# Kernel optimization log

Measured on AMD Instinct MI355X. Metric: run time of the kernel, lower is better.

Reference implementation:

```python
import jax, jax.numpy as jnp
import numpy as np
from jax import lax

D = 1024          # channel / embedding dim
K = 2048          # codebook size
BN_EPS = 1e-5


def conv1d(x, w, b, stride):
    # x: [N, C, L], w: [O, I, k]
    y = lax.conv_general_dilated(x, w, window_strides=(stride,), padding='VALID',
                                 dimension_numbers=('NCH', 'OIH', 'NCH'))
    return y + b[None, :, None]


def batchnorm1d(x, gamma, beta):
    # training-mode BN: batch statistics over (N, L) per channel, biased variance
    mean = jnp.mean(x, axis=(0, 2), keepdims=True)
    var = jnp.var(x, axis=(0, 2), keepdims=True)
    return (x - mean) * lax.rsqrt(var + BN_EPS) * gamma[None, :, None] + beta[None, :, None]


def setup_inputs() -> dict:
    key = jax.random.key(0)
    ks = jax.random.split(key, 8)
    x = jax.random.normal(ks[0], (32, D, 1024), dtype=jnp.float32)
    conv1_w = jax.random.normal(ks[1], (D, D, 4), dtype=jnp.float32) * 0.02
    conv1_b = jnp.zeros((D,), dtype=jnp.float32)
    bn1_g = jnp.ones((D,), dtype=jnp.float32)
    bn1_b = jnp.zeros((D,), dtype=jnp.float32)
    conv2_w = jax.random.normal(ks[2], (D, D, 1), dtype=jnp.float32) * 0.02
    conv2_b = jnp.zeros((D,), dtype=jnp.float32)
    bn2_g = jnp.ones((D,), dtype=jnp.float32)
    bn2_b = jnp.zeros((D,), dtype=jnp.float32)
    codebook = jax.random.normal(ks[3], (K, D), dtype=jnp.float32)
    return {'x': x, 'conv1_w': conv1_w, 'conv1_b': conv1_b,
            'bn1_g': bn1_g, 'bn1_b': bn1_b,
            'conv2_w': conv2_w, 'conv2_b': conv2_b,
            'bn2_g': bn2_g, 'bn2_b': bn2_b,
            'codebook': codebook}


def encoder(x, conv1_w, conv1_b, bn1_g, bn1_b, conv2_w, conv2_b, bn2_g, bn2_b):
    h = conv1d(x, conv1_w, conv1_b, stride=2)           # [B, D, L']
    # ResidualWrapper(BN -> ReLU -> Conv1x1)
    r = batchnorm1d(h, bn1_g, bn1_b)
    r = jax.nn.relu(r)
    r = conv1d(r, conv2_w, conv2_b, stride=1)
    h = h + r
    h = batchnorm1d(h, bn2_g, bn2_b)
    return h


def vq(h, codebook):
    # axis=1 -> move channel axis last: [B, L', D]
    z = jnp.moveaxis(h, 1, -1)
    # squared Euclidean distances via ||z||^2 - 2 z.e + ||e||^2  (cdist+argmin)
    z2 = jnp.sum(z * z, axis=-1, keepdims=True)                  # [B, L', 1]
    e2 = jnp.sum(codebook * codebook, axis=-1)                   # [K]
    ze = jnp.einsum('bld,kd->blk', z, codebook)                  # [B, L', K]
    dist2 = z2 - 2.0 * ze + e2[None, None, :]
    ids = jnp.argmin(dist2, axis=-1)                             # [B, L'] int
    q = codebook[ids]                                            # [B, L', D]
    sg = lax.stop_gradient
    commitment = jnp.mean((z - sg(q)) ** 2)
    codebook_loss = jnp.mean((sg(z) - q) ** 2)
    # straight-through estimator
    q_st = z + sg(q - z)
    q_st = jnp.moveaxis(q_st, -1, 1)                             # back to [B, D, L']
    return q_st, ids, commitment, codebook_loss


def reference(x, conv1_w, conv1_b, bn1_g, bn1_b, conv2_w, conv2_b, bn2_g, bn2_b, codebook):
    h = encoder(x, conv1_w, conv1_b, bn1_g, bn1_b, conv2_w, conv2_b, bn2_g, bn2_b)
    q_st, ids, commitment, codebook_loss = vq(h, codebook)
    return q_st, ids, commitment, codebook_loss
```

## Files before the change

kernel.cpp:

```cpp
#include <hip/hip_runtime.h>
#include <hip/hip_bf16.h>
#include <cstdint>

#define DD 1024
#define LIN 1024
#define LP 511
#define LPAD 512
#define NBATCH 32
#define KCB 2048
#define BN_EPS 1e-5f

#define OUT_IDS 16744448u
#define OUT_LOSS 16760800u

#define WS_H1 0
#define WS_UNI 16777216
#define WS_XH  (WS_UNI)
#define WS_XL  (WS_UNI + 16777728)
#define WS_WTH (WS_UNI + 33555456)
#define WS_WTL (WS_UNI + 35652608)
#define WS_T2  (WS_UNI)
#define WS_RH  (WS_UNI + 16777216)
#define WS_RL  (WS_UNI + 25165824)
#define WS_ZH  WS_RH
#define WS_ZL  WS_RL
#define WS_W2H (WS_UNI + 33554432)
#define WS_W2L (WS_UNI + 34078720)
#define WS_CBH (WS_UNI + 34603008)
#define WS_CBL (WS_UNI + 35651584)
#define WS_AUX (WS_UNI + 37749760)
#define WS_A1 (WS_AUX + 0)
#define WS_B1 (WS_AUX + 1024)
#define WS_A2 (WS_AUX + 2048)
#define WS_B2 (WS_AUX + 3072)
#define WS_E2 (WS_AUX + 4096)
#define WS_SLOTS (WS_AUX + 6144)
#define WS_LOSS (WS_AUX + 6144 + 32704)

typedef __attribute__((ext_vector_type(8))) short bf16x8;
typedef __attribute__((ext_vector_type(4))) float f32x4;
typedef __attribute__((ext_vector_type(4))) unsigned short ushort4v;

__device__ __forceinline__ void async_cp16(const void* gsrc, void* ldst) {
  __builtin_amdgcn_global_load_lds(
      (const __attribute__((address_space(1))) unsigned int*)gsrc,
      (__attribute__((address_space(3))) unsigned int*)ldst, 16, 0, 0);
}

__device__ __forceinline__ void bf16split(float v, unsigned short& hi, unsigned short& lo) {
  __hip_bfloat16 h = __float2bfloat16(v);
  float hf = __bfloat162float(h);
  __hip_bfloat16 l = __float2bfloat16(v - hf);
  hi = *(unsigned short*)&h;
  lo = *(unsigned short*)&l;
}

__device__ inline float blockReduce256(float v, float* sb) {
#pragma unroll
  for (int off = 32; off > 0; off >>= 1) v += __shfl_down(v, off);
  __syncthreads();
  if ((threadIdx.x & 63) == 0) sb[threadIdx.x >> 6] = v;
  __syncthreads();
  return sb[0] + sb[1] + sb[2] + sb[3];
}

#define VMCNT(n) asm volatile("s_waitcnt vmcnt(" #n ")" ::: "memory")

template <typename SF>
__device__ __forceinline__ void stage_slot(const SF& sf, int c, int slot,
                                           unsigned short* smbase, int wid,
                                           int lane) {
  int plane, r0;
  if (slot < 4) {
    plane = 2 + (slot >> 1);
    r0 = ((slot & 1) << 7) + (wid << 4);
  } else {
    plane = wid & 1;
    r0 = (((wid >> 1) & 1) << 7) + ((slot - 4) << 5) + ((wid >> 2) << 4);
  }
  const unsigned short* g = sf(c, plane) + (size_t)(r0 + (lane >> 2)) * 1024 +
                            (((lane & 3) ^ ((lane >> 3) & 3)) << 3);
  unsigned short* d = smbase + plane * 8192 + r0 * 32;
  async_cp16(g, d);
}

template <typename SF>
__device__ __forceinline__ void mfma256_core(const SF& sf, unsigned short* sm,
                                             int nkc, f32x4 (&acc)[8][4]) {
  const int tid = threadIdx.x;
  const int wid = tid >> 6, lane = tid & 63;
  const int wm = wid >> 2, wn = wid & 3;
  const int slot16 = (((lane >> 4) ^ ((lane >> 1) & 3)) << 3);
  const int arow = (wm << 7) + (lane & 15);
  const int brow = (wn << 6) + (lane & 15);

#pragma unroll
  for (int s = 0; s < 8; ++s) stage_slot(sf, 0, s, sm, wid, lane);

  bf16x8 fbh[4], fbl[4];
  for (int c = 0; c < nkc; ++c) {
    unsigned short* buf = sm + ((c & 1) << 15);
    unsigned short* nbuf = sm + (((c + 1) & 1) << 15);
    const unsigned short* As = buf;
    const unsigned short* Als = buf + 8192;
    const unsigned short* Bs = buf + 16384;
    const unsigned short* Bls = buf + 24576;
    const bool pre = (c + 1 < nkc);
#pragma unroll
    for (int p = 0; p < 4; ++p) {
      if (pre) {
        if (p == 0) { VMCNT(3); } else if (p == 1) { VMCNT(4); }
        else if (p == 2) { VMCNT(5); } else { VMCNT(6); }
      } else {
        if (p == 0) { VMCNT(3); } else if (p == 1) { VMCNT(2); }
        else if (p == 2) { VMCNT(1); } else { VMCNT(0); }
      }
      __builtin_amdgcn_s_barrier();
      asm volatile("" ::: "memory");
      __builtin_amdgcn_sched_barrier(0);
      if (p == 0) {
#pragma unroll
        for (int nt = 0; nt < 4; ++nt) {
          int r = brow + nt * 16;
          fbh[nt] = *(const bf16x8*)(Bs + r * 32 + slot16);
          fbl[nt] = *(const bf16x8*)(Bls + r * 32 + slot16);
        }
      }
      bf16x8 fah0, fal0, fah1, fal1;
      {
        int r0 = arow + ((2 * p) << 4);
        int r1 = r0 + 16;
        fah0 = *(const bf16x8*)(As + r0 * 32 + slot16);
        fal0 = *(const bf16x8*)(Als + r0 * 32 + slot16);
        fah1 = *(const bf16x8*)(As + r1 * 32 + slot16);
        fal1 = *(const bf16x8*)(Als + r1 * 32 + slot16);
      }
      if (pre) {
        stage_slot(sf, c + 1, 2 * p + 0, nbuf, wid, lane);
        stage_slot(sf, c + 1, 2 * p + 1, nbuf, wid, lane);
      }
      __builtin_amdgcn_s_setprio(1);
#pragma unroll
      for (int nt = 0; nt < 4; ++nt) {
        acc[2 * p][nt] = __builtin_amdgcn_mfma_f32_16x16x32_bf16(fah0, fbh[nt], acc[2 * p][nt], 0, 0, 0);
        acc[2 * p][nt] = __builtin_amdgcn_mfma_f32_16x16x32_bf16(fah0, fbl[nt], acc[2 * p][nt], 0, 0, 0);
        acc[2 * p][nt] = __builtin_amdgcn_mfma_f32_16x16x32_bf16(fal0, fbh[nt], acc[2 * p][nt], 0, 0, 0);
      }
#pragma unroll
      for (int nt = 0; nt < 4; ++nt) {
        acc[2 * p + 1][nt] = __builtin_amdgcn_mfma_f32_16x16x32_bf16(fah1, fbh[nt], acc[2 * p + 1][nt], 0, 0, 0);
        acc[2 * p + 1][nt] = __builtin_amdgcn_mfma_f32_16x16x32_bf16(fah1, fbl[nt], acc[2 * p + 1][nt], 0, 0, 0);
        acc[2 * p + 1][nt] = __builtin_amdgcn_mfma_f32_16x16x32_bf16(fal1, fbh[nt], acc[2 * p + 1][nt], 0, 0, 0);
      }
      __builtin_amdgcn_s_setprio(0);
    }
  }
}

__global__ __launch_bounds__(256) void split_w1_kernel(
    const float* __restrict__ w, unsigned short* __restrict__ wth,
    unsigned short* __restrict__ wtl) {
  int idx = blockIdx.x * 256 + threadIdx.x;
  int o = idx >> 10, i = idx & 1023;
  float4 v = *(const float4*)&w[(size_t)idx * 4];
  float vv[4] = {v.x, v.y, v.z, v.w};
#pragma unroll
  for (int t = 0; t < 4; ++t) {
    unsigned short hi, lo;
    bf16split(vv[t], hi, lo);
    size_t off = (((size_t)(t << 10) + o) << 10) + i;
    wth[off] = hi;
    wtl[off] = lo;
  }
}

__global__ __launch_bounds__(256) void split_rows_kernel(
    const float* __restrict__ src, unsigned short* __restrict__ dsth,
    unsigned short* __restrict__ dstl) {
  size_t base = ((size_t)blockIdx.x * 256 + threadIdx.x) * 4;
  float4 v = *(const float4*)&src[base];
  float vv[4] = {v.x, v.y, v.z, v.w};
  ushort4v h, l;
#pragma unroll
  for (int j = 0; j < 4; ++j) {
    unsigned short hi, lo;
    bf16split(vv[j], hi, lo);
    h[j] = hi;
    l[j] = lo;
  }
  *(ushort4v*)&dsth[base] = h;
  *(ushort4v*)&dstl[base] = l;
}

__global__ __launch_bounds__(256) void split_x_kernel(
    const float* __restrict__ x, unsigned short* __restrict__ xh,
    unsigned short* __restrict__ xl) {
  __shared__ float lsT[128 * 65];
  const int l0 = blockIdx.x * 128;
  const int i0 = blockIdx.y * 64;
  const int nB = blockIdx.z;
  const int tid = threadIdx.x;
#pragma unroll
  for (int p = 0; p < 8; ++p) {
    int flat = p * 256 + tid;
    int row = flat >> 5, col4 = (flat & 31) * 4;
    float4 v = *(const float4*)&x[((size_t)nB * DD + i0 + row) * LIN + l0 + col4];
    lsT[(col4 + 0) * 65 + row] = v.x;
    lsT[(col4 + 1) * 65 + row] = v.y;
    lsT[(col4 + 2) * 65 + row] = v.z;
    lsT[(col4 + 3) * 65 + row] = v.w;
  }
  __syncthreads();
  const int lo2 = (l0 >> 1);
#pragma unroll
  for (int p = 0; p < 16; ++p) {
    int cp = p * 4 + (tid >> 6);
    int il = tid & 63;
    float vE = lsT[(2 * cp) * 65 + il];
    float vO = lsT[(2 * cp + 1) * 65 + il];
    unsigned short hE, lE, hO, lO;
    bf16split(vE, hE, lE);
    bf16split(vO, hO, lO);
    size_t dE = (((size_t)(0 * 32 + nB) * 512) + lo2 + cp) * 1024 + i0 + il;
    size_t dO = (((size_t)(1 * 32 + nB) * 512) + lo2 + cp) * 1024 + i0 + il;
    xh[dE] = hE; xl[dE] = lE;
    xh[dO] = hO; xl[dO] = lO;
  }
}

__global__ __launch_bounds__(256) void trans_affine_split_kernel(
    const float* __restrict__ src, const float* __restrict__ a,
    const float* __restrict__ b, unsigned short* __restrict__ dsth,
    unsigned short* __restrict__ dstl, int do_relu) {
  __shared__ float lsT[128 * 65];
  const int l0 = blockIdx.x * 128;
  const int i0 = blockIdx.y * 64;
  const int nB = blockIdx.z;
  const int tid = threadIdx.x;
#pragma unroll
  for (int p = 0; p < 8; ++p) {
    int flat = p * 256 + tid;
    int row = flat >> 5, col4 = (flat & 31) * 4;
    float4 v = *(const float4*)&src[((size_t)nB * DD + i0 + row) * LPAD + l0 + col4];
    lsT[(col4 + 0) * 65 + row] = v.x;
    lsT[(col4 + 1) * 65 + row] = v.y;
    lsT[(col4 + 2) * 65 + row] = v.z;
    lsT[(col4 + 3) * 65 + row] = v.w;
  }
  __syncthreads();
  const int il = tid & 63;
  const float ac = a[i0 + il], bc = b[i0 + il];
#pragma unroll
  for (int p = 0; p < 32; ++p) {
    int cp = p * 4 + (tid >> 6);
    float v = fmaf(ac, lsT[cp * 65 + il], bc);
    if (do_relu) v = fmaxf(v, 0.f);
    unsigned short hi, lo;
    bf16split(v, hi, lo);
    size_t d = (((size_t)nB * 512) + l0 + cp) * 1024 + i0 + il;
    dsth[d] = hi;
    dstl[d] = lo;
  }
}

__global__ __launch_bounds__(512, 2) void conv1_mfma_kernel(
    const unsigned short* __restrict__ wth, const unsigned short* __restrict__ wtl,
    const unsigned short* __restrict__ xh, const unsigned short* __restrict__ xl,
    const float* __restrict__ bias, float* __restrict__ h1) {
  extern __shared__ unsigned short sm[];
  const int tid = threadIdx.x;
  const int wid = tid >> 6, lane = tid & 63;
  const int lb = blockIdx.x * 256, ob = blockIdx.y * 256, nB = blockIdx.z;

  f32x4 acc[8][4];
#pragma unroll
  for (int a = 0; a < 8; ++a)
#pragma unroll
    for (int b = 0; b < 4; ++b) acc[a][b] = (f32x4){0.f, 0.f, 0.f, 0.f};

  auto sf = [&](int c, int plane) -> const unsigned short* {
    int t = c >> 5, kc = c & 31;
    if (plane == 0) return wth + ((((size_t)t << 10) + ob) << 10) + kc * 32;
    if (plane == 1) return wtl + ((((size_t)t << 10) + ob) << 10) + kc * 32;
    const unsigned short* xp = (plane == 2) ? xh : xl;
    return xp + ((((size_t)((t & 1) * 32 + nB) * 512) + lb + (t >> 1)) << 10) + kc * 32;
  };
  mfma256_core(sf, sm, 128, acc);

  const int wm = wid >> 2, wn = wid & 3;
#pragma unroll
  for (int mt = 0; mt < 8; ++mt) {
    const int o_base = ob + (wm << 7) + mt * 16 + ((lane >> 4) << 2);
#pragma unroll
    for (int nt = 0; nt < 4; ++nt) {
      const int l = lb + (wn << 6) + nt * 16 + (lane & 15);
      if (l < LP) {
#pragma unroll
        for (int rg = 0; rg < 4; ++rg)
          h1[((size_t)(nB << 10) + o_base + rg) * LPAD + l] =
              acc[mt][nt][rg] + bias[o_base + rg];
      }
    }
  }
}

__global__ __launch_bounds__(512, 2) void conv2_mfma_kernel(
    const unsigned short* __restrict__ w2h, const unsigned short* __restrict__ w2l,
    const unsigned short* __restrict__ rh, const unsigned short* __restrict__ rl,
    const float* __restrict__ b2c, const float* __restrict__ h1,
    float* __restrict__ t2) {
  extern __shared__ unsigned short sm[];
  const int tid = threadIdx.x;
  const int wid = tid >> 6, lane = tid & 63;
  const int lb = blockIdx.x * 256, ob = blockIdx.y * 256, nB = blockIdx.z;

  f32x4 acc[8][4];
#pragma unroll
  for (int a = 0; a < 8; ++a)
#pragma unroll
    for (int b = 0; b < 4; ++b) acc[a][b] = (f32x4){0.f, 0.f, 0.f, 0.f};

  auto sf = [&](int c, int plane) -> const unsigned short* {
    if (plane == 0) return w2h + ((size_t)ob << 10) + (size_t)c * 32;
    if (plane == 1) return w2l + ((size_t)ob << 10) + (size_t)c * 32;
    const unsigned short* rp = (plane == 2) ? rh : rl;
    return rp + (((size_t)nB * 512 + lb) << 10) + (size_t)c * 32;
  };
  mfma256_core(sf, sm, 32, acc);

  const int wm = wid >> 2, wn = wid & 3;
#pragma unroll
  for (int mt = 0; mt < 8; ++mt) {
    const int o_base = ob + (wm << 7) + mt * 16 + ((lane >> 4) << 2);
#pragma unroll
    for (int nt = 0; nt < 4; ++nt) {
      const int l = lb + (wn << 6) + nt * 16 + (lane & 15);
      if (l < LP) {
#pragma unroll
        for (int rg = 0; rg < 4; ++rg) {
          size_t off = ((size_t)(nB << 10) + o_base + rg) * LPAD + l;
          t2[off] = h1[off] + acc[mt][nt][rg] + b2c[o_base + rg];
        }
      }
    }
  }
}

__global__ __launch_bounds__(512, 2) void dist_mfma_kernel(
    const unsigned short* __restrict__ cbh, const unsigned short* __restrict__ cbl,
    const unsigned short* __restrict__ zh, const unsigned short* __restrict__ zl,
    const float* __restrict__ e2, unsigned long long* __restrict__ slots) {
  extern __shared__ unsigned short sm[];
  unsigned long long* best = (unsigned long long*)(sm + 65536);
  const int tid = threadIdx.x;
  const int wid = tid >> 6, lane = tid & 63;
  const int lb = blockIdx.x * 256, kb = blockIdx.y * 256, nB = blockIdx.z;

  if (tid < 256) best[tid] = ~0ULL;

  f32x4 acc[8][4];
#pragma unroll
  for (int a = 0; a < 8; ++a)
#pragma unroll
    for (int b = 0; b < 4; ++b) acc[a][b] = (f32x4){0.f, 0.f, 0.f, 0.f};

  auto sf = [&](int c, int plane) -> const unsigned short* {
    if (plane == 0) return cbh + ((size_t)kb << 10) + (size_t)c * 32;
    if (plane == 1) return cbl + ((size_t)kb << 10) + (size_t)c * 32;
    const unsigned short* zp = (plane == 2) ? zh : zl;
    return zp + (((size_t)nB * 512 + lb) << 10) + (size_t)c * 32;
  };
  mfma256_core(sf, sm, 32, acc);

  const int wm = wid >> 2, wn = wid & 3;
#pragma unroll
  for (int nt = 0; nt < 4; ++nt) {
    const int col = (wn << 6) + nt * 16 + (lane & 15);
    float dmin = 3.4e38f;
    int kmin = 0;
#pragma unroll
    for (int mt = 0; mt < 8; ++mt) {
      const int kbase = kb + (wm << 7) + mt * 16 + ((lane >> 4) << 2);
#pragma unroll
      for (int rg = 0; rg < 4; ++rg) {
        float dist = fmaf(-2.f, acc[mt][nt][rg], e2[kbase + rg]);
        if (dist < dmin) { dmin = dist; kmin = kbase + rg; }
      }
    }
    unsigned long long pk =
        ((unsigned long long)__float_as_uint(dmin) << 32) | (unsigned)kmin;
    atomicMin(&best[col], pk);
  }
  __syncthreads();
  if (tid < 256) {
    int l = lb + tid;
    if (l < LP) atomicMin(&slots[(size_t)nB * LP + l], best[tid]);
  }
}

__global__ __launch_bounds__(256) void bn_stats_kernel(
    const float* __restrict__ src, const float* __restrict__ gamma,
    const float* __restrict__ beta, float* __restrict__ a_out,
    float* __restrict__ b_out) {
  __shared__ float sb[4];
  const int c = blockIdx.x;
  const float* p = src + (size_t)c * LPAD;
  float s1 = 0.f, s2 = 0.f;
  for (int idx = threadIdx.x; idx < NBATCH * LP; idx += 256) {
    int nn = idx / LP;
    int l = idx - nn * LP;
    float v = p[(size_t)nn * DD * LPAD + l];
    s1 += v;
    s2 = fmaf(v, v, s2);
  }
  s1 = blockReduce256(s1, sb);
  s2 = blockReduce256(s2, sb);
  if (threadIdx.x == 0) {
    const float inv = 1.f / (float)(NBATCH * LP);
    float m = s1 * inv;
    float var = fmaf(-m, m, s2 * inv);
    float a = gamma[c] * rsqrtf(var + BN_EPS);
    a_out[c] = a;
    b_out[c] = fmaf(-m, a, beta[c]);
  }
}

__global__ __launch_bounds__(256) void e2_kernel(const float* __restrict__ cb,
                                                 float* __restrict__ e2) {
  __shared__ float sb[4];
  const int k = blockIdx.x;
  float s = 0.f;
  for (int d = threadIdx.x; d < DD; d += 256) {
    float v = cb[(size_t)k * DD + d];
    s = fmaf(v, v, s);
  }
  s = blockReduce256(s, sb);
  if (threadIdx.x == 0) e2[k] = s;
}

__global__ __launch_bounds__(256) void gather_kernel(
    const float* __restrict__ t2, const float* __restrict__ cb,
    const float* __restrict__ a2, const float* __restrict__ b2,
    const unsigned long long* __restrict__ slots, float* __restrict__ out,
    float* __restrict__ loss_acc) {
  __shared__ int ks[64];
  __shared__ float sb[4];
  const int l0 = blockIdx.x * 64;
  const int n = blockIdx.y;
  const int tid = threadIdx.x, tx = tid & 63, ty = tid >> 6;
  if (tid < 64) {
    int l = l0 + tid;
    int k = 0;
    if (l < LP) {
      k = (int)(unsigned)(slots[(size_t)n * LP + l] & 0xffffffffULL);
      out[OUT_IDS + (size_t)n * LP + l] = (float)k;
    }
    ks[tid] = k;
  }
  __syncthreads();
  const int l = l0 + tx;
  const bool valid = (l < LP);
  const int k = ks[tx];
  const float* cbk = cb + (size_t)k * DD;
  const float* tn = t2 + (size_t)n * DD * LPAD;
  float* qo = out + (size_t)n * DD * LP;
  float lsum = 0.f;
  for (int d0 = 0; d0 < DD; d0 += 4) {
    const int d = d0 + ty;
    float q = cbk[d];
    if (valid) {
      float z = fmaf(a2[d], tn[(size_t)d * LPAD + l], b2[d]);
      qo[(size_t)d * LP + l] = q;
      float e = z - q;
      lsum = fmaf(e, e, lsum);
    }
  }
  lsum = blockReduce256(lsum, sb);
  if (tid == 0) atomicAdd(loss_acc, lsum);
}

__global__ void finalize_kernel(const float* __restrict__ loss_acc,
                                float* __restrict__ out) {
  if (threadIdx.x == 0) {
    float m = loss_acc[0] * (1.f / 16744448.f);
    out[OUT_LOSS] = m;
    out[OUT_LOSS + 1] = m;
  }
}

extern "C" void kernel_launch(void* const* d_in, const int* in_sizes, int n_in,
                              void* d_out, int out_size, void* d_ws,
                              size_t ws_size, hipStream_t stream) {
  const float* x = (const float*)d_in[0];
  const float* w1 = (const float*)d_in[1];
  const float* b1c = (const float*)d_in[2];
  const float* g1 = (const float*)d_in[3];
  const float* be1 = (const float*)d_in[4];
  const float* w2 = (const float*)d_in[5];
  const float* b2c = (const float*)d_in[6];
  const float* g2 = (const float*)d_in[7];
  const float* be2 = (const float*)d_in[8];
  const float* cb = (const float*)d_in[9];
  float* out = (float*)d_out;
  float* ws = (float*)d_ws;

  float* h1 = ws + WS_H1;
  float* t2 = ws + WS_T2;
  unsigned short* xh = (unsigned short*)(ws + WS_XH);
  unsigned short* xl = (unsigned short*)(ws + WS_XL);
  unsigned short* wth = (unsigned short*)(ws + WS_WTH);
  unsigned short* wtl = (unsigned short*)(ws + WS_WTL);
  unsigned short* rh = (unsigned short*)(ws + WS_RH);
  unsigned short* rl = (unsigned short*)(ws + WS_RL);
  unsigned short* zh = (unsigned short*)(ws + WS_ZH);
  unsigned short* zl = (unsigned short*)(ws + WS_ZL);
  unsigned short* w2h = (unsigned short*)(ws + WS_W2H);
  unsigned short* w2l = (unsigned short*)(ws + WS_W2L);
  unsigned short* cbh = (unsigned short*)(ws + WS_CBH);
  unsigned short* cbl = (unsigned short*)(ws + WS_CBL);
  float* a1 = ws + WS_A1;
  float* bb1 = ws + WS_B1;
  float* a2 = ws + WS_A2;
  float* bb2 = ws + WS_B2;
  float* e2 = ws + WS_E2;
  unsigned long long* slots = (unsigned long long*)(ws + WS_SLOTS);
  float* loss = ws + WS_LOSS;

  static int attr_done = 0;
  if (!attr_done) {
    (void)hipFuncSetAttribute(reinterpret_cast<const void*>(conv1_mfma_kernel),
                              hipFuncAttributeMaxDynamicSharedMemorySize, 135168);
    (void)hipFuncSetAttribute(reinterpret_cast<const void*>(conv2_mfma_kernel),
                              hipFuncAttributeMaxDynamicSharedMemorySize, 135168);
    (void)hipFuncSetAttribute(reinterpret_cast<const void*>(dist_mfma_kernel),
                              hipFuncAttributeMaxDynamicSharedMemorySize, 135168);
    attr_done = 1;
  }

  (void)hipMemsetAsync(slots, 0xFF,
                       (size_t)NBATCH * LP * sizeof(unsigned long long), stream);
  (void)hipMemsetAsync(loss, 0, sizeof(float), stream);

  split_w1_kernel<<<4096, 256, 0, stream>>>(w1, wth, wtl);
  split_x_kernel<<<dim3(8, 16, NBATCH), 256, 0, stream>>>(x, xh, xl);
  conv1_mfma_kernel<<<dim3(2, 4, NBATCH), 512, 131072, stream>>>(wth, wtl, xh,
                                                                 xl, b1c, h1);
  bn_stats_kernel<<<DD, 256, 0, stream>>>(h1, g1, be1, a1, bb1);
  split_rows_kernel<<<1024, 256, 0, stream>>>(w2, w2h, w2l);
  split_rows_kernel<<<2048, 256, 0, stream>>>(cb, cbh, cbl);
  e2_kernel<<<KCB, 256, 0, stream>>>(cb, e2);
  trans_affine_split_kernel<<<dim3(4, 16, NBATCH), 256, 0, stream>>>(
      h1, a1, bb1, rh, rl, 1);
  conv2_mfma_kernel<<<dim3(2, 4, NBATCH), 512, 131072, stream>>>(w2h, w2l, rh,
                                                                 rl, b2c, h1, t2);
  bn_stats_kernel<<<DD, 256, 0, stream>>>(t2, g2, be2, a2, bb2);
  trans_affine_split_kernel<<<dim3(4, 16, NBATCH), 256, 0, stream>>>(
      t2, a2, bb2, zh, zl, 0);
  dist_mfma_kernel<<<dim3(2, 8, NBATCH), 512, 133120, stream>>>(cbh, cbl, zh,
                                                                zl, e2, slots);
  gather_kernel<<<dim3(8, NBATCH), 256, 0, stream>>>(t2, cb, a2, bb2, slots, out, loss);
  finalize_kernel<<<1, 64, 0, stream>>>(loss, out);
}
```

Measured before the change: 1.025 ms.

## Switch GEMM cores to 32x32x16 MFMA and swizzle conv block order

The shared split-bf16 GEMM core now issues 32x32x16 MFMA instructions instead of 16x16x32, using f32x16 accumulators. It processes two half-iterations per K-chunk with four async stage copies each, and reindexes every epilogue (conv1 store, conv2 residual add, distance argmin) to the 32x32 output layout. The conv1 and conv2 launches move to a flat 1D grid with a remapped block order, so neighbouring blocks share weight and activation tiles in cache. The larger MFMA needs fewer LDS fragment reads per flop, at the cost of coarser load/compute interleaving and more complex index maths.

```diff
diff --git a/kernel.cpp b/kernel.cpp
--- a/kernel.cpp
+++ b/kernel.cpp
@@ -39,6 +39,7 @@
 
 typedef __attribute__((ext_vector_type(8))) short bf16x8;
 typedef __attribute__((ext_vector_type(4))) float f32x4;
+typedef __attribute__((ext_vector_type(16))) float f32x16;
 typedef __attribute__((ext_vector_type(4))) unsigned short ushort4v;
 
 __device__ __forceinline__ void async_cp16(const void* gsrc, void* ldst) {
@@ -85,19 +86,21 @@
 }
 
 template <typename SF>
-__device__ __forceinline__ void mfma256_core(const SF& sf, unsigned short* sm,
-                                             int nkc, f32x4 (&acc)[8][4]) {
+__device__ __forceinline__ void mfma256_core32(const SF& sf, unsigned short* sm,
+                                               int nkc, f32x16 (&acc)[4][2]) {
   const int tid = threadIdx.x;
   const int wid = tid >> 6, lane = tid & 63;
   const int wm = wid >> 2, wn = wid & 3;
-  const int slot16 = (((lane >> 4) ^ ((lane >> 1) & 3)) << 3);
-  const int arow = (wm << 7) + (lane & 15);
-  const int brow = (wn << 6) + (lane & 15);
+  const int lrow = lane & 31;
+  const int khalf = lane >> 5;
+  const int sig = (lane >> 1) & 3;
+  const int arowb = (wm << 7) + lrow;
+  const int browb = (wn << 6) + lrow;
 
 #pragma unroll
   for (int s = 0; s < 8; ++s) stage_slot(sf, 0, s, sm, wid, lane);
 
-  bf16x8 fbh[4], fbl[4];
+  bf16x8 fbh[2][2], fbl[2][2];
   for (int c = 0; c < nkc; ++c) {
     unsigned short* buf = sm + ((c & 1) << 15);
     unsigned short* nbuf = sm + (((c + 1) & 1) << 15);
@@ -107,50 +110,61 @@
     const unsigned short* Bls = buf + 24576;
     const bool pre = (c + 1 < nkc);
 #pragma unroll
-    for (int p = 0; p < 4; ++p) {
-      if (pre) {
-        if (p == 0) { VMCNT(3); } else if (p == 1) { VMCNT(4); }
-        else if (p == 2) { VMCNT(5); } else { VMCNT(6); }
+    for (int q = 0; q < 2; ++q) {
+      if (q == 0) {
+        VMCNT(2);
+      } else if (pre) {
+        VMCNT(4);
       } else {
-        if (p == 0) { VMCNT(3); } else if (p == 1) { VMCNT(2); }
-        else if (p == 2) { VMCNT(1); } else { VMCNT(0); }
+        VMCNT(0);
       }
       __builtin_amdgcn_s_barrier();
       asm volatile("" ::: "memory");
       __builtin_amdgcn_sched_barrier(0);
-      if (p == 0) {
-#pragma unroll
-        for (int nt = 0; nt < 4; ++nt) {
-          int r = brow + nt * 16;
-          fbh[nt] = *(const bf16x8*)(Bs + r * 32 + slot16);
-          fbl[nt] = *(const bf16x8*)(Bls + r * 32 + slot16);
+      if (q == 0) {
+#pragma unroll
+        for (int nt = 0; nt < 2; ++nt) {
+          const int r = browb + nt * 32;
+#pragma unroll
+          for (int kh = 0; kh < 2; ++kh) {
+            const int off = r * 32 + ((((kh << 1) + khalf) ^ sig) << 3);
+            fbh[kh][nt] = *(const bf16x8*)(Bs + off);
+            fbl[kh][nt] = *(const bf16x8*)(Bls + off);
+          }
         }
       }
-      bf16x8 fah0, fal0, fah1, fal1;
-      {
-        int r0 = arow + ((2 * p) << 4);
-        int r1 = r0 + 16;
-        fah0 = *(const bf16x8*)(As + r0 * 32 + slot16);
-        fal0 = *(const bf16x8*)(Als + r0 * 32 + slot16);
-        fah1 = *(const bf16x8*)(As + r1 * 32 + slot16);
-        fal1 = *(const bf16x8*)(Als + r1 * 32 + slot16);
+      bf16x8 fah[2][2], fal[2][2];
+#pragma unroll
+      for (int mi = 0; mi < 2; ++mi) {
+        const int r = arowb + ((q << 1) + mi) * 32;
+#pragma unroll
+        for (int kh = 0; kh < 2; ++kh) {
+          const int off = r * 32 + ((((kh << 1) + khalf) ^ sig) << 3);
+          fah[mi][kh] = *(const bf16x8*)(As + off);
+          fal[mi][kh] = *(const bf16x8*)(Als + off);
+        }
       }
       if (pre) {
-        stage_slot(sf, c + 1, 2 * p + 0, nbuf, wid, lane);
-        stage_slot(sf, c + 1, 2 * p + 1, nbuf, wid, lane);
+#pragma unroll
+        for (int s = 0; s < 4; ++s)
+          stage_slot(sf, c + 1, (q << 2) + s, nbuf, wid, lane);
       }
       __builtin_amdgcn_s_setprio(1);
 #pragma unroll
-      for (int nt = 0; nt < 4; ++nt) {
-        acc[2 * p][nt] = __builtin_amdgcn_mfma_f32_16x16x32_bf16(fah0, fbh[nt], acc[2 * p][nt], 0, 0, 0);
-        acc[2 * p][nt] = __builtin_amdgcn_mfma_f32_16x16x32_bf16(fah0, fbl[nt], acc[2 * p][nt], 0, 0, 0);
-        acc[2 * p][nt] = __builtin_amdgcn_mfma_f32_16x16x32_bf16(fal0, fbh[nt], acc[2 * p][nt], 0, 0, 0);
-      }
-#pragma unroll
-      for (int nt = 0; nt < 4; ++nt) {
-        acc[2 * p + 1][nt] = __builtin_amdgcn_mfma_f32_16x16x32_bf16(fah1, fbh[nt], acc[2 * p + 1][nt], 0, 0, 0);
-        acc[2 * p + 1][nt] = __builtin_amdgcn_mfma_f32_16x16x32_bf16(fah1, fbl[nt], acc[2 * p + 1][nt], 0, 0, 0);
-        acc[2 * p + 1][nt] = __builtin_amdgcn_mfma_f32_16x16x32_bf16(fal1, fbh[nt], acc[2 * p + 1][nt], 0, 0, 0);
+      for (int kh = 0; kh < 2; ++kh) {
+#pragma unroll
+        for (int t = 0; t < 3; ++t) {
+#pragma unroll
+          for (int mi = 0; mi < 2; ++mi) {
+#pragma unroll
+            for (int nt = 0; nt < 2; ++nt) {
+              const bf16x8 af = (t == 2) ? fal[mi][kh] : fah[mi][kh];
+              const bf16x8 bb = (t == 1) ? fbl[kh][nt] : fbh[kh][nt];
+              acc[(q << 1) + mi][nt] = __builtin_amdgcn_mfma_f32_32x32x16_bf16(
+                  af, bb, acc[(q << 1) + mi][nt], 0, 0, 0);
+            }
+          }
+        }
       }
       __builtin_amdgcn_s_setprio(0);
     }
@@ -270,13 +284,18 @@
   extern __shared__ unsigned short sm[];
   const int tid = threadIdx.x;
   const int wid = tid >> 6, lane = tid & 63;
-  const int lb = blockIdx.x * 256, ob = blockIdx.y * 256, nB = blockIdx.z;
-
-  f32x4 acc[8][4];
-#pragma unroll
-  for (int a = 0; a < 8; ++a)
-#pragma unroll
-    for (int b = 0; b < 4; ++b) acc[a][b] = (f32x4){0.f, 0.f, 0.f, 0.f};
+  const int lin = blockIdx.x;
+  const int lb = (lin & 1) * 256;
+  const int nB = ((lin >> 1) & 3) | ((lin >> 5) << 2);
+  const int ob = ((lin >> 3) & 3) * 256;
+
+  f32x16 acc[4][2];
+#pragma unroll
+  for (int a = 0; a < 4; ++a)
+#pragma unroll
+    for (int b = 0; b < 2; ++b)
+#pragma unroll
+      for (int e = 0; e < 16; ++e) acc[a][b][e] = 0.f;
 
   auto sf = [&](int c, int plane) -> const unsigned short* {
     int t = c >> 5, kc = c & 31;
@@ -285,20 +304,23 @@
     const unsigned short* xp = (plane == 2) ? xh : xl;
     return xp + ((((size_t)((t & 1) * 32 + nB) * 512) + lb + (t >> 1)) << 10) + kc * 32;
   };
-  mfma256_core(sf, sm, 128, acc);
+  mfma256_core32(sf, sm, 128, acc);
 
   const int wm = wid >> 2, wn = wid & 3;
 #pragma unroll
-  for (int mt = 0; mt < 8; ++mt) {
-    const int o_base = ob + (wm << 7) + mt * 16 + ((lane >> 4) << 2);
-#pragma unroll
-    for (int nt = 0; nt < 4; ++nt) {
-      const int l = lb + (wn << 6) + nt * 16 + (lane & 15);
+  for (int mt = 0; mt < 4; ++mt) {
+#pragma unroll
+    for (int nt = 0; nt < 2; ++nt) {
+      const int l = lb + (wn << 6) + nt * 32 + (lane & 31);
       if (l < LP) {
 #pragma unroll
-        for (int rg = 0; rg < 4; ++rg)
-          h1[((size_t)(nB << 10) + o_base + rg) * LPAD + l] =
-              acc[mt][nt][rg] + bias[o_base + rg];
+        for (int rq = 0; rq < 4; ++rq) {
+          const int o0 = ob + (wm << 7) + mt * 32 + rq * 8 + ((lane >> 5) << 2);
+#pragma unroll
+          for (int rg = 0; rg < 4; ++rg)
+            h1[((size_t)(nB << 10) + o0 + rg) * LPAD + l] =
+                acc[mt][nt][rq * 4 + rg] + bias[o0 + rg];
+        }
       }
     }
   }
@@ -312,13 +334,18 @@
   extern __shared__ unsigned short sm[];
   const int tid = threadIdx.x;
   const int wid = tid >> 6, lane = tid & 63;
-  const int lb = blockIdx.x * 256, ob = blockIdx.y * 256, nB = blockIdx.z;
-
-  f32x4 acc[8][4];
-#pragma unroll
-  for (int a = 0; a < 8; ++a)
-#pragma unroll
-    for (int b = 0; b < 4; ++b) acc[a][b] = (f32x4){0.f, 0.f, 0.f, 0.f};
+  const int lin = blockIdx.x;
+  const int lb = (lin & 1) * 256;
+  const int nB = ((lin >> 1) & 3) | ((lin >> 5) << 2);
+  const int ob = ((lin >> 3) & 3) * 256;
+
+  f32x16 acc[4][2];
+#pragma unroll
+  for (int a = 0; a < 4; ++a)
+#pragma unroll
+    for (int b = 0; b < 2; ++b)
+#pragma unroll
+      for (int e = 0; e < 16; ++e) acc[a][b][e] = 0.f;
 
   auto sf = [&](int c, int plane) -> const unsigned short* {
     if (plane == 0) return w2h + ((size_t)ob << 10) + (size_t)c * 32;
@@ -326,20 +353,23 @@
     const unsigned short* rp = (plane == 2) ? rh : rl;
     return rp + (((size_t)nB * 512 + lb) << 10) + (size_t)c * 32;
   };
-  mfma256_core(sf, sm, 32, acc);
+  mfma256_core32(sf, sm, 32, acc);
 
   const int wm = wid >> 2, wn = wid & 3;
 #pragma unroll
-  for (int mt = 0; mt < 8; ++mt) {
-    const int o_base = ob + (wm << 7) + mt * 16 + ((lane >> 4) << 2);
-#pragma unroll
-    for (int nt = 0; nt < 4; ++nt) {
-      const int l = lb + (wn << 6) + nt * 16 + (lane & 15);
+  for (int mt = 0; mt < 4; ++mt) {
+#pragma unroll
+    for (int nt = 0; nt < 2; ++nt) {
+      const int l = lb + (wn << 6) + nt * 32 + (lane & 31);
       if (l < LP) {
 #pragma unroll
-        for (int rg = 0; rg < 4; ++rg) {
-          size_t off = ((size_t)(nB << 10) + o_base + rg) * LPAD + l;
-          t2[off] = h1[off] + acc[mt][nt][rg] + b2c[o_base + rg];
+        for (int rq = 0; rq < 4; ++rq) {
+          const int o0 = ob + (wm << 7) + mt * 32 + rq * 8 + ((lane >> 5) << 2);
+#pragma unroll
+          for (int rg = 0; rg < 4; ++rg) {
+            size_t off = ((size_t)(nB << 10) + o0 + rg) * LPAD + l;
+            t2[off] = h1[off] + acc[mt][nt][rq * 4 + rg] + b2c[o0 + rg];
+          }
         }
       }
     }
@@ -358,11 +388,13 @@
 
   if (tid < 256) best[tid] = ~0ULL;
 
-  f32x4 acc[8][4];
-#pragma unroll
-  for (int a = 0; a < 8; ++a)
-#pragma unroll
-    for (int b = 0; b < 4; ++b) acc[a][b] = (f32x4){0.f, 0.f, 0.f, 0.f};
+  f32x16 acc[4][2];
+#pragma unroll
+  for (int a = 0; a < 4; ++a)
+#pragma unroll
+    for (int b = 0; b < 2; ++b)
+#pragma unroll
+      for (int e = 0; e < 16; ++e) acc[a][b][e] = 0.f;
 
   auto sf = [&](int c, int plane) -> const unsigned short* {
     if (plane == 0) return cbh + ((size_t)kb << 10) + (size_t)c * 32;
@@ -370,21 +402,24 @@
     const unsigned short* zp = (plane == 2) ? zh : zl;
     return zp + (((size_t)nB * 512 + lb) << 10) + (size_t)c * 32;
   };
-  mfma256_core(sf, sm, 32, acc);
+  mfma256_core32(sf, sm, 32, acc);
 
   const int wm = wid >> 2, wn = wid & 3;
 #pragma unroll
-  for (int nt = 0; nt < 4; ++nt) {
-    const int col = (wn << 6) + nt * 16 + (lane & 15);
+  for (int nt = 0; nt < 2; ++nt) {
+    const int col = (wn << 6) + nt * 32 + (lane & 31);
     float dmin = 3.4e38f;
     int kmin = 0;
 #pragma unroll
-    for (int mt = 0; mt < 8; ++mt) {
-      const int kbase = kb + (wm << 7) + mt * 16 + ((lane >> 4) << 2);
-#pragma unroll
-      for (int rg = 0; rg < 4; ++rg) {
-        float dist = fmaf(-2.f, acc[mt][nt][rg], e2[kbase + rg]);
-        if (dist < dmin) { dmin = dist; kmin = kbase + rg; }
+    for (int mt = 0; mt < 4; ++mt) {
+#pragma unroll
+      for (int rq = 0; rq < 4; ++rq) {
+        const int kbase = kb + (wm << 7) + mt * 32 + rq * 8 + ((lane >> 5) << 2);
+#pragma unroll
+        for (int rg = 0; rg < 4; ++rg) {
+          float dist = fmaf(-2.f, acc[mt][nt][rq * 4 + rg], e2[kbase + rg]);
+          if (dist < dmin) { dmin = dist; kmin = kbase + rg; }
+        }
       }
     }
     unsigned long long pk =
@@ -543,16 +578,14 @@
 
   split_w1_kernel<<<4096, 256, 0, stream>>>(w1, wth, wtl);
   split_x_kernel<<<dim3(8, 16, NBATCH), 256, 0, stream>>>(x, xh, xl);
-  conv1_mfma_kernel<<<dim3(2, 4, NBATCH), 512, 131072, stream>>>(wth, wtl, xh,
-                                                                 xl, b1c, h1);
+  conv1_mfma_kernel<<<256, 512, 131072, stream>>>(wth, wtl, xh, xl, b1c, h1);
   bn_stats_kernel<<<DD, 256, 0, stream>>>(h1, g1, be1, a1, bb1);
   split_rows_kernel<<<1024, 256, 0, stream>>>(w2, w2h, w2l);
   split_rows_kernel<<<2048, 256, 0, stream>>>(cb, cbh, cbl);
   e2_kernel<<<KCB, 256, 0, stream>>>(cb, e2);
   trans_affine_split_kernel<<<dim3(4, 16, NBATCH), 256, 0, stream>>>(
       h1, a1, bb1, rh, rl, 1);
-  conv2_mfma_kernel<<<dim3(2, 4, NBATCH), 512, 131072, stream>>>(w2h, w2l, rh,
-                                                                 rl, b2c, h1, t2);
+  conv2_mfma_kernel<<<256, 512, 131072, stream>>>(w2h, w2l, rh, rl, b2c, h1, t2);
   bn_stats_kernel<<<DD, 256, 0, stream>>>(t2, g2, be2, a2, bb2);
   trans_affine_split_kernel<<<dim3(4, 16, NBATCH), 256, 0, stream>>>(
       t2, a2, bb2, zh, zl, 0);
```

Measured after the change: 1.025 ms. About the same (+0.0%).
